# Performance work log

Hardware: AMD Instinct MI355X
Metric: run time of the kernel (lower is better)

Reference implementation:

```python
import jax, jax.numpy as jnp
import numpy as np

B, N, E, D = 8, 10000, 160000, 256
H = D // 2
SLOPE = 0.2  # LeakyReLU negative slope


def setup_inputs() -> dict:
    key = jax.random.key(0)
    ks = jax.random.split(key, 8)
    node_feats = jax.random.normal(ks[0], (B, N, D), dtype=jnp.float32)
    edge_attr = jax.random.uniform(ks[1], (E, 1), dtype=jnp.float32)
    W1 = jax.random.normal(ks[2], (2 * D, H), dtype=jnp.float32) * 0.05
    b1 = jnp.zeros((H,), dtype=jnp.float32)
    W2 = jax.random.normal(ks[3], (H, 1), dtype=jnp.float32) * 0.05
    b2 = jnp.zeros((1,), dtype=jnp.float32)
    edge_index = jax.random.randint(ks[4], (2, E), 0, N, dtype=jnp.int64)
    valid_masks = jax.random.randint(ks[5], (B, N), 0, 2).astype(bool)
    return {"node_feats": node_feats, "edge_attr": edge_attr, "W1": W1, "b1": b1,
            "W2": W2, "b2": b2, "edge_index": edge_index, "valid_masks": valid_masks}


def reference(node_feats, edge_attr, W1, b1, W2, b2, edge_index, valid_masks):
    # node_feats: [B,N,D]; edge_index: [2,E] shared across batch
    d = node_feats.shape[-1]
    src, dst = edge_index[0], edge_index[1]
    # cat([src_feats, dst_feats]) @ W1 == src @ W1[:d] + dst @ W1[d:]
    # Project per-node first, then gather per-edge: avoids the [B,E,2D] concat.
    ps = jnp.einsum('bnd,dh->bnh', node_feats, W1[:d])   # [B,N,H]
    pd = jnp.einsum('bnd,dh->bnh', node_feats, W1[d:])   # [B,N,H]
    h = ps[:, src] + pd[:, dst] + b1                      # [B,E,H]
    h = jnp.where(h >= 0, h, SLOPE * h)                   # LeakyReLU(0.2)
    scores = jnp.einsum('beh,h->be', h, W2[:, 0]) + b2[0]  # [B,E]
    scores = scores * edge_attr[:, 0]                     # edge_attr multiplies pre-softmax
    w = jax.nn.softmax(scores, axis=1)                    # global softmax over all edges
    # sparse_coo(edge_index, w) @ node_feats: out[src[e]] += w[e] * feats[dst[e]]
    msg = w[..., None] * node_feats[:, dst]               # [B,E,D]
    n = node_feats.shape[1]
    agg = jax.vmap(lambda m: jax.ops.segment_sum(m, src, num_segments=n))(msg)  # [B,N,D]
    mask = valid_masks.astype(node_feats.dtype)           # [B,N]
    cnt = mask.sum(axis=1)                                # [B]
    masked_mean = (agg * mask[..., None]).sum(axis=1) / jnp.maximum(cnt, 1.0)[:, None]
    full_mean = agg.mean(axis=1)
    graph_feats = jnp.where((cnt > 0)[:, None], masked_mean, full_mean)  # [B,D]
    return graph_feats, w
```

## Files before the change

kernel.cpp:

```cpp
#include <hip/hip_runtime.h>
#include <hip/hip_bf16.h>
#include <hip/hip_fp16.h>

#define B_ 8
#define N_ 10000
#define E_ 160000
#define D_ 256
#define H_ 128
#define SLOPE 0.2f
#define NCHUNK 50

#define EC_ 16
#define NR_ 32
#define RANGE_ 320
#define NPAD_ (NR_ * RANGE_)

#define NB_ 64
#define EPB_ (E_ / NB_)
#define BINS_ 256
#define NPB_ (N_ / 16)

typedef __attribute__((ext_vector_type(8))) _Float16 v8h;
typedef __attribute__((ext_vector_type(4))) _Float16 v4h;
typedef __attribute__((ext_vector_type(2))) _Float16 v2h;
typedef __attribute__((ext_vector_type(4))) float f32x4;

static __device__ __forceinline__ float dot2f(v2h a, v2h b, float c) {
#if __has_builtin(__builtin_amdgcn_fdot2)
    return __builtin_amdgcn_fdot2(a, b, c, false);
#else
    return fmaf((float)a.y, (float)b.y, fmaf((float)a.x, (float)b.x, c));
#endif
}

__global__ __launch_bounds__(64) void k_detect(const int* __restrict__ eidx_raw,
                                               const unsigned int* __restrict__ mask32,
                                               int* __restrict__ flags) {
    const int t = threadIdx.x;
    unsigned long long oddnz = __ballot(eidx_raw[2 * t + 1] != 0);
    unsigned long long mgt1  = __ballot(mask32[t] > 1u);
    if (t == 0) {
        flags[0] = (oddnz == 0ull) ? 1 : 0;
        flags[1] = (mgt1 != 0ull) ? 1 : 0;
    }
}

__global__ __launch_bounds__(256) void k_canon(const int* __restrict__ eidx_raw,
                                               const unsigned char* __restrict__ mask8,
                                               const unsigned int* __restrict__ mask32,
                                               const int* __restrict__ flags,
                                               int* __restrict__ ce,
                                               unsigned char* __restrict__ cm,
                                               unsigned char* __restrict__ cmT) {
    const int i = blockIdx.x * 256 + threadIdx.x;
    const int f_e = flags[0], f_m = flags[1];
    if (i < 2 * E_) ce[i] = f_e ? eidx_raw[2 * i] : eidx_raw[i];
    if (i < B_ * N_) {
        unsigned char v = f_m ? (unsigned char)(mask8[i] != 0)
                              : (unsigned char)(mask32[i] != 0u);
        cm[i] = v;
        const int b = i / N_;
        const int n = i - b * N_;
        cmT[n * 8 + b] = v;
    }
}

__global__ __launch_bounds__(256) void kW(const float* __restrict__ W1,
                                          const float* __restrict__ b1,
                                          const float* __restrict__ W2,
                                          __half* __restrict__ Wt,
                                          __half* __restrict__ b1h,
                                          __half* __restrict__ w2h) {
    const int i = blockIdx.x * 256 + threadIdx.x;
    const int f = i & 127;
    const int row = i >> 7;
    const int c = row >> 8, k = row & 255;
    Wt[((c * 128 + f) * 256) + k] = __float2half(W1[row * 128 + f]);
    if (blockIdx.x == 0 && threadIdx.x < 128) {
        b1h[threadIdx.x] = __float2half(b1[threadIdx.x]);
        w2h[threadIdx.x] = __float2half(W2[threadIdx.x]);
    }
}

__global__ __launch_bounds__(256) void k0_init(const unsigned char* __restrict__ cm,
                                               float* __restrict__ cnt) {
    const int b = blockIdx.x;
    const int tid = threadIdx.x;
    int c = 0;
    for (int i = tid; i < N_; i += 256) c += cm[b * N_ + i] ? 1 : 0;
    __shared__ int red[256];
    red[tid] = c;
    __syncthreads();
    for (int s = 128; s > 0; s >>= 1) {
        if (tid < s) red[tid] += red[tid + s];
        __syncthreads();
    }
    if (tid == 0) cnt[b] = (float)red[0];
}

__global__ __launch_bounds__(256) void khist(const int* __restrict__ ce,
                                             int* __restrict__ hpart) {
    __shared__ int h[BINS_];
    const int tid = threadIdx.x;
    h[tid] = 0;
    __syncthreads();
    const int base = blockIdx.x * EPB_;
    for (int i = tid; i < EPB_; i += 256) {
        const int s = ce[base + i], d = ce[E_ + base + i];
        const int bin = (d / NPB_) * 16 + s / NPB_;
        atomicAdd(&h[bin], 1);
    }
    __syncthreads();
    hpart[blockIdx.x * BINS_ + tid] = h[tid];
}

__global__ __launch_bounds__(256) void kprefix(const int* __restrict__ hpart,
                                               int* __restrict__ offsetG) {
    __shared__ int cnt[BINS_];
    __shared__ int excl[BINS_];
    const int bin = threadIdx.x;
    int c = 0;
    for (int b = 0; b < NB_; b++) c += hpart[b * BINS_ + bin];
    cnt[bin] = c;
    __syncthreads();
    if (bin == 0) {
        int r = 0;
        for (int i = 0; i < BINS_; i++) { excl[i] = r; r += cnt[i]; }
    }
    __syncthreads();
    int run = excl[bin];
    for (int b = 0; b < NB_; b++) {
        offsetG[b * BINS_ + bin] = run;
        run += hpart[b * BINS_ + bin];
    }
}

__global__ __launch_bounds__(256) void kscatter(const int* __restrict__ ce,
                                                const int* __restrict__ offsetG,
                                                int* __restrict__ srcS,
                                                int* __restrict__ dstS,
                                                int* __restrict__ origS) {
    __shared__ int loc[BINS_];
    const int tid = threadIdx.x;
    loc[tid] = offsetG[blockIdx.x * BINS_ + tid];
    __syncthreads();
    const int base = blockIdx.x * EPB_;
    for (int i = tid; i < EPB_; i += 256) {
        const int e = base + i;
        const int s = ce[e], d = ce[E_ + e];
        const int bin = (d / NPB_) * 16 + s / NPB_;
        const int pos = atomicAdd(&loc[bin], 1);
        srcS[pos] = s;
        dstS[pos] = d;
        origS[pos] = e;
    }
}

__global__ __launch_bounds__(256) void k1_mfma(const float* __restrict__ X,
                                               const __half* __restrict__ Wt,
                                               __half* __restrict__ ps,
                                               __half* __restrict__ pd) {
    const int cb = blockIdx.y;
    const int rb = blockIdx.x;
    const int tid = threadIdx.x;
    const int wave = tid >> 6, lane = tid & 63;
    const int quad = lane >> 4, l16 = lane & 15;

    __shared__ _Float16 Xs[128 * 40];
    __shared__ _Float16 Ws[128 * 40];

    f32x4 acc[2][8];
#pragma unroll
    for (int i = 0; i < 2; i++)
#pragma unroll
        for (int j = 0; j < 8; j++) acc[i][j] = (f32x4){0.f, 0.f, 0.f, 0.f};

    const int row_base = rb * 128;
    const __half* __restrict__ Wh = Wt + (size_t)cb * 128 * 256;
    __half* __restrict__ outp = cb ? pd : ps;

    const int sr = tid >> 1;
    const int sh = tid & 1;

    for (int kc = 0; kc < 8; ++kc) {
        {
            const float4* src = (const float4*)&X[(size_t)(row_base + sr) * 256 + kc * 32 + sh * 16];
            _Float16* dst = &Xs[sr * 40 + sh * 16];
#pragma unroll
            for (int j = 0; j < 4; ++j) {
                float4 v = src[j];
                v4h p = {(_Float16)v.x, (_Float16)v.y, (_Float16)v.z, (_Float16)v.w};
                *(v4h*)&dst[j * 4] = p;
            }
        }
        {
            const float4* src = (const float4*)&Wh[(size_t)sr * 256 + kc * 32 + sh * 16];
            float4 v0 = src[0], v1 = src[1];
            *(float4*)&Ws[sr * 40 + sh * 16] = v0;
            *(float4*)&Ws[sr * 40 + sh * 16 + 8] = v1;
        }
        __syncthreads();

        v8h wf[2];
#pragma unroll
        for (int ft = 0; ft < 2; ++ft)
            wf[ft] = *(v8h*)&Ws[(wave * 32 + ft * 16 + l16) * 40 + quad * 8];
#pragma unroll
        for (int nt = 0; nt < 8; ++nt) {
            v8h xf = *(v8h*)&Xs[(nt * 16 + l16) * 40 + quad * 8];
            acc[0][nt] = __builtin_amdgcn_mfma_f32_16x16x32_f16(wf[0], xf, acc[0][nt], 0, 0, 0);
            acc[1][nt] = __builtin_amdgcn_mfma_f32_16x16x32_f16(wf[1], xf, acc[1][nt], 0, 0, 0);
        }
        __syncthreads();
    }

#pragma unroll
    for (int nt = 0; nt < 8; ++nt) {
        const int R = row_base + nt * 16 + l16;
        const int b = R / N_;
        const int n = R - b * N_;
        __half* base = outp + ((size_t)(n * 8 + b)) * 128 + wave * 32 + quad * 4;
#pragma unroll
        for (int ft = 0; ft < 2; ++ft) {
            f32x4 a = acc[ft][nt];
            v4h h = {(_Float16)a.x, (_Float16)a.y, (_Float16)a.z, (_Float16)a.w};
            *(v4h*)(base + ft * 16) = h;
        }
    }
}

__global__ __launch_bounds__(256) void k2_scores(const __half* __restrict__ ps,
                                                 const __half* __restrict__ pd,
                                                 const int* __restrict__ srcS,
                                                 const int* __restrict__ dstS,
                                                 const int* __restrict__ origS,
                                                 const __half* __restrict__ b1h,
                                                 const __half* __restrict__ w2h,
                                                 const float* __restrict__ b2,
                                                 const float* __restrict__ eattr,
                                                 float* __restrict__ scores) {
    const int tid = threadIdx.x;
    const int wave = tid >> 6;
    const int lane = tid & 63;
    const int bid = blockIdx.x;
    const int lb = (bid & 7) * 5000 + (bid >> 3);
    const int e = lb * 4 + wave;

    const int b = lane >> 3;
    const int hi = (lane & 7) * 16;

    v2h b1p[8], w2p[8];
    {
        const v2h* bp = (const v2h*)(b1h + hi);
        const v2h* wp = (const v2h*)(w2h + hi);
#pragma unroll
        for (int j = 0; j < 8; j++) { b1p[j] = bp[j]; w2p[j] = wp[j]; }
    }

    const int src = srcS[e];
    const int dst = dstS[e];
    const int orig = origS[e];

    const float4* aps = (const float4*)&ps[((size_t)src * 8 + b) * 128 + hi];
    const float4* apd = (const float4*)&pd[((size_t)dst * 8 + b) * 128 + hi];
    float4 rs[2] = {aps[0], aps[1]};
    float4 rd[2] = {apd[0], apd[1]};
    const v2h* sv = (const v2h*)rs;
    const v2h* dv = (const v2h*)rd;

    const v2h slp = {(_Float16)SLOPE, (_Float16)SLOPE};
    float acc = 0.f;
#pragma unroll
    for (int j = 0; j < 8; j++) {
        v2h x = sv[j] + dv[j] + b1p[j];
        v2h l = __builtin_elementwise_max(x, x * slp);
        acc = dot2f(l, w2p[j], acc);
    }
    acc += __shfl_xor(acc, 1);
    acc += __shfl_xor(acc, 2);
    acc += __shfl_xor(acc, 4);

    if ((lane & 7) == 0) {
        scores[(size_t)b * E_ + orig] = (acc + b2[0]) * eattr[orig];
    }
}

__global__ __launch_bounds__(256) void k3a_max(const float* __restrict__ sc,
                                               float* __restrict__ pmax) {
    const int b = blockIdx.y, c = blockIdx.x, tid = threadIdx.x;
    const float* x = sc + (size_t)b * E_;
    const int i0 = c * (E_ / 32);
    float mv = -3.4e38f;
    for (int i = i0 + tid; i < i0 + E_ / 32; i += 256) mv = fmaxf(mv, x[i]);
    __shared__ float red[256];
    red[tid] = mv;
    __syncthreads();
    for (int s = 128; s > 0; s >>= 1) {
        if (tid < s) red[tid] = fmaxf(red[tid], red[tid + s]);
        __syncthreads();
    }
    if (tid == 0) pmax[b * 32 + c] = red[0];
}

__global__ __launch_bounds__(256) void k3b_maxred(const float* __restrict__ pmax,
                                                  float* __restrict__ m) {
    const int t = threadIdx.x;
    float v = pmax[t];
#pragma unroll
    for (int k = 1; k <= 16; k <<= 1) v = fmaxf(v, __shfl_xor(v, k));
    if ((t & 31) == 0) m[t >> 5] = v;
}

__global__ __launch_bounds__(256) void k3c_sum(const float* __restrict__ sc,
                                               const float* __restrict__ m,
                                               double* __restrict__ psum) {
    const int b = blockIdx.y, c = blockIdx.x, tid = threadIdx.x;
    const float* x = sc + (size_t)b * E_;
    const float mv = m[b];
    const int i0 = c * (E_ / 32);
    double s = 0.0;
    for (int i = i0 + tid; i < i0 + E_ / 32; i += 256) s += (double)expf(x[i] - mv);
    __shared__ double red[256];
    red[tid] = s;
    __syncthreads();
    for (int st = 128; st > 0; st >>= 1) {
        if (tid < st) red[tid] += red[tid + st];
        __syncthreads();
    }
    if (tid == 0) psum[b * 32 + c] = red[0];
}

__global__ __launch_bounds__(256) void k3d_sumred(const double* __restrict__ psum,
                                                  float* __restrict__ inv) {
    const int t = threadIdx.x;
    double v = psum[t];
#pragma unroll
    for (int k = 1; k <= 16; k <<= 1) v += __shfl_xor(v, k);
    if ((t & 31) == 0) inv[t >> 5] = (float)(1.0 / v);
}

__global__ __launch_bounds__(256) void k3e_norm(float* __restrict__ sc,
                                                const float* __restrict__ m,
                                                const float* __restrict__ inv,
                                                float* __restrict__ wT) {
    const int e = blockIdx.x * 256 + threadIdx.x;
    float wv[8];
#pragma unroll
    for (int b = 0; b < 8; b++) {
        float v = expf(sc[(size_t)b * E_ + e] - m[b]) * inv[b];
        sc[(size_t)b * E_ + e] = v;
        wv[b] = v;
    }
    *(float4*)&wT[(size_t)e * 8]     = make_float4(wv[0], wv[1], wv[2], wv[3]);
    *(float4*)&wT[(size_t)e * 8 + 4] = make_float4(wv[4], wv[5], wv[6], wv[7]);
}

__global__ __launch_bounds__(256) void k3f_bin(const int* __restrict__ ce,
                                               const float* __restrict__ wT,
                                               const unsigned char* __restrict__ cmT,
                                               float* __restrict__ Wpart) {
    const int ec = blockIdx.x;
    const int rg = blockIdx.y;
    const int n0 = rg * RANGE_;

    __shared__ float lWf[RANGE_ * 8];
    __shared__ float lWm[RANGE_ * 8];
    for (int i = threadIdx.x; i < RANGE_ * 8; i += 256) { lWf[i] = 0.f; lWm[i] = 0.f; }
    __syncthreads();

    const int4* dst4 = (const int4*)(ce + E_);
    const int base4 = ec * (E_ / EC_ / 4);
    for (int i = threadIdx.x; i < E_ / EC_ / 4; i += 256) {
        int4 d4 = dst4[base4 + i];
        int dd[4] = {d4.x, d4.y, d4.z, d4.w};
        const int e0 = (base4 + i) * 4;
#pragma unroll
        for (int j = 0; j < 4; ++j) {
            const int rel = dd[j] - n0;
            if ((unsigned)rel < (unsigned)RANGE_) {
                const int e = e0 + j;
                const int src = ce[e];
                float4 w0 = *(const float4*)&wT[(size_t)e * 8];
                float4 w1 = *(const float4*)&wT[(size_t)e * 8 + 4];
                const unsigned long long mm = *(const unsigned long long*)&cmT[src * 8];
                float wv[8] = {w0.x, w0.y, w0.z, w0.w, w1.x, w1.y, w1.z, w1.w};
                float* lf = &lWf[rel * 8];
                float* lm = &lWm[rel * 8];
#pragma unroll
                for (int b = 0; b < 8; b++) {
                    atomicAdd(&lf[b], wv[b]);
                    if ((mm >> (8 * b)) & 1ull) atomicAdd(&lm[b], wv[b]);
                }
            }
        }
    }
    __syncthreads();

    float* of = Wpart + ((size_t)ec * 2 + 0) * (NPAD_ * 8) + n0 * 8;
    float* om = Wpart + ((size_t)ec * 2 + 1) * (NPAD_ * 8) + n0 * 8;
    for (int i = threadIdx.x; i < RANGE_ * 8; i += 256) { of[i] = lWf[i]; om[i] = lWm[i]; }
}

__global__ __launch_bounds__(256) void k3g_reduce(const float* __restrict__ Wpart,
                                                  float* __restrict__ WfT,
                                                  float* __restrict__ WmT) {
    const int i = blockIdx.x * 256 + threadIdx.x;
    float sf = 0.f, sm = 0.f;
#pragma unroll
    for (int ec = 0; ec < EC_; ec++) {
        sf += Wpart[(size_t)ec * 2 * (NPAD_ * 8) + i];
        sm += Wpart[((size_t)ec * 2 + 1) * (NPAD_ * 8) + i];
    }
    WfT[i] = sf;
    WmT[i] = sm;
}

__global__ __launch_bounds__(256) void k4b_wsum(const float* __restrict__ X,
                                                const float* __restrict__ WmT,
                                                const float* __restrict__ WfT,
                                                float* __restrict__ gpart) {
    const int c = blockIdx.x;
    const int b = blockIdx.y;
    const int tx = threadIdx.x & 63;
    const int ty = threadIdx.x >> 6;
    const int npc = N_ / NCHUNK;
    const int n0 = c * npc;

    const float4* X4 = (const float4*)(X + (size_t)b * N_ * 256);
    float4 am = {0.f, 0.f, 0.f, 0.f};
    float4 af = {0.f, 0.f, 0.f, 0.f};

    for (int n = n0 + ty; n < n0 + npc; n += 4) {
        float wm = WmT[n * 8 + b];
        float wf = WfT[n * 8 + b];
        float4 v = X4[(size_t)n * 64 + tx];
        am.x = fmaf(wm, v.x, am.x); am.y = fmaf(wm, v.y, am.y);
        am.z = fmaf(wm, v.z, am.z); am.w = fmaf(wm, v.w, am.w);
        af.x = fmaf(wf, v.x, af.x); af.y = fmaf(wf, v.y, af.y);
        af.z = fmaf(wf, v.z, af.z); af.w = fmaf(wf, v.w, af.w);
    }

    __shared__ float4 red[256];
    red[threadIdx.x] = am;
    __syncthreads();
    if (ty == 0) {
        float4 r1 = red[tx + 64], r2 = red[tx + 128], r3 = red[tx + 192];
        am.x += r1.x + r2.x + r3.x; am.y += r1.y + r2.y + r3.y;
        am.z += r1.z + r2.z + r3.z; am.w += r1.w + r2.w + r3.w;
    }
    __syncthreads();
    red[threadIdx.x] = af;
    __syncthreads();
    if (ty == 0) {
        float4 r1 = red[tx + 64], r2 = red[tx + 128], r3 = red[tx + 192];
        af.x += r1.x + r2.x + r3.x; af.y += r1.y + r2.y + r3.y;
        af.z += r1.z + r2.z + r3.z; af.w += r1.w + r2.w + r3.w;
        float4* gp4 = (float4*)gpart;
        gp4[((c * 2 + 0) * 8 + b) * 64 + tx] = am;
        gp4[((c * 2 + 1) * 8 + b) * 64 + tx] = af;
    }
}

__global__ __launch_bounds__(256) void k5_final(const float* __restrict__ gpart,
                                                const float* __restrict__ cnt,
                                                float* __restrict__ gf) {
    const int b = blockIdx.x;
    const int d = threadIdx.x;
    float sm = 0.f, sf = 0.f;
    for (int c = 0; c < NCHUNK; c++) {
        sm += gpart[((c * 2 + 0) * 8 + b) * 256 + d];
        sf += gpart[((c * 2 + 1) * 8 + b) * 256 + d];
    }
    const float cn = cnt[b];
    gf[b * 256 + d] = (cn > 0.f) ? (sm / cn) : (sf / (float)N_);
}

extern "C" void kernel_launch(void* const* d_in, const int* in_sizes, int n_in,
                              void* d_out, int out_size, void* d_ws, size_t ws_size,
                              hipStream_t stream) {
    const float* X     = (const float*)d_in[0];
    const float* eattr = (const float*)d_in[1];
    const float* W1    = (const float*)d_in[2];
    const float* b1    = (const float*)d_in[3];
    const float* W2    = (const float*)d_in[4];
    const float* b2    = (const float*)d_in[5];
    const int*   eidx_raw = (const int*)d_in[6];
    const unsigned char* mask8 = (const unsigned char*)d_in[7];
    const unsigned int*  mask32 = (const unsigned int*)d_in[7];

    float* out  = (float*)d_out;
    float* gf   = out;
    float* wout = out + 2048;

    __half* ps_h = (__half*)d_ws;
    __half* pd_h = ps_h + (size_t)N_ * 8 * 128;
    __half* Wt   = pd_h + (size_t)N_ * 8 * 128;
    int* ce = (int*)(Wt + 2 * 128 * 256);
    unsigned char* cmT = (unsigned char*)(ce + 2 * E_);
    unsigned char* cm  = cmT + NPAD_ * 8;
    float* cnt = (float*)(cm + B_ * N_);
    int* flags = (int*)(cnt + 8);
    float* pmax = (float*)(flags + 2);
    float* mbuf = pmax + 256;
    float* invb = mbuf + 8;
    double* psum = (double*)(((uintptr_t)(invb + 8) + 15) & ~(uintptr_t)15);
    float* gpart = (float*)(psum + 256);
    int* hpart   = (int*)(gpart + NCHUNK * 2 * 8 * 256);
    int* offsetG = hpart + NB_ * BINS_;
    int* srcS    = offsetG + NB_ * BINS_;
    int* dstS    = srcS + E_;
    int* origS   = dstS + E_;
    __half* b1h  = (__half*)(origS + E_);
    __half* w2h  = b1h + 128;

    float* wT    = (float*)d_ws;
    float* Wpart = wT + (size_t)E_ * 8;
    float* WfT   = Wpart + (size_t)EC_ * 2 * NPAD_ * 8;
    float* WmT   = WfT + NPAD_ * 8;

    hipLaunchKernelGGL(k_detect, dim3(1), dim3(64), 0, stream, eidx_raw, mask32, flags);
    hipLaunchKernelGGL(k_canon, dim3(1250), dim3(256), 0, stream,
                       eidx_raw, mask8, mask32, flags, ce, cm, cmT);
    hipLaunchKernelGGL(kW, dim3(256), dim3(256), 0, stream, W1, b1, W2, Wt, b1h, w2h);
    hipLaunchKernelGGL(k0_init, dim3(8), dim3(256), 0, stream, cm, cnt);
    hipLaunchKernelGGL(khist, dim3(NB_), dim3(256), 0, stream, ce, hpart);
    hipLaunchKernelGGL(kprefix, dim3(1), dim3(256), 0, stream, hpart, offsetG);
    hipLaunchKernelGGL(kscatter, dim3(NB_), dim3(256), 0, stream,
                       ce, offsetG, srcS, dstS, origS);
    hipLaunchKernelGGL(k1_mfma, dim3(625, 2), dim3(256), 0, stream, X, Wt, ps_h, pd_h);
    hipLaunchKernelGGL(k2_scores, dim3(E_ / 4), dim3(256), 0, stream,
                       ps_h, pd_h, srcS, dstS, origS, b1h, w2h, b2, eattr, wout);
    hipLaunchKernelGGL(k3a_max, dim3(32, 8), dim3(256), 0, stream, wout, pmax);
    hipLaunchKernelGGL(k3b_maxred, dim3(1), dim3(256), 0, stream, pmax, mbuf);
    hipLaunchKernelGGL(k3c_sum, dim3(32, 8), dim3(256), 0, stream, wout, mbuf, psum);
    hipLaunchKernelGGL(k3d_sumred, dim3(1), dim3(256), 0, stream, psum, invb);
    hipLaunchKernelGGL(k3e_norm, dim3(E_ / 256), dim3(256), 0, stream,
                       wout, mbuf, invb, wT);
    hipLaunchKernelGGL(k3f_bin, dim3(EC_, NR_), dim3(256), 0, stream, ce, wT, cmT, Wpart);
    hipLaunchKernelGGL(k3g_reduce, dim3(NPAD_ * 8 / 256), dim3(256), 0, stream,
                       Wpart, WfT, WmT);
    hipLaunchKernelGGL(k4b_wsum, dim3(NCHUNK, 8), dim3(256), 0, stream, X, WmT, WfT, gpart);
    hipLaunchKernelGGL(k5_final, dim3(8), dim3(256), 0, stream, gpart, cnt, gf);
}
```

Before: 324.5 us.

## Fuse small setup kernels, merge GEMM column blocks, and restructure softmax reductions

Folds the weight conversion into the canonicalisation kernel and the mask count into the histogram kernel. The two projection GEMM column blocks become one block that reuses the staged X tile, with W fragments read straight from global memory instead of shared memory. Scores are now stored in sorted-edge order, interleaved across the batch, so the max and sum passes read them with coalesced vector loads. The separate reduction kernels are folded into their consumers, and a rank array lets the normalize pass map each edge back to its sorted position. This cuts the number of launches and scattered stores, at the cost of a gather through rank in the normalize pass and more GEMM registers.

```diff
diff --git a/kernel.cpp b/kernel.cpp
--- a/kernel.cpp
+++ b/kernel.cpp
@@ -19,6 +19,9 @@
 #define EPB_ (E_ / NB_)
 #define BINS_ 256
 #define NPB_ (N_ / 16)
+
+#define SB_ 64
+#define SEB_ (E_ / SB_)
 
 typedef __attribute__((ext_vector_type(8))) _Float16 v8h;
 typedef __attribute__((ext_vector_type(4))) _Float16 v4h;
@@ -49,9 +52,15 @@
                                                const unsigned char* __restrict__ mask8,
                                                const unsigned int* __restrict__ mask32,
                                                const int* __restrict__ flags,
+                                               const float* __restrict__ W1,
+                                               const float* __restrict__ b1,
+                                               const float* __restrict__ W2,
                                                int* __restrict__ ce,
                                                unsigned char* __restrict__ cm,
-                                               unsigned char* __restrict__ cmT) {
+                                               unsigned char* __restrict__ cmT,
+                                               __half* __restrict__ Wt,
+                                               __half* __restrict__ b1h,
+                                               __half* __restrict__ w2h) {
     const int i = blockIdx.x * 256 + threadIdx.x;
     const int f_e = flags[0], f_m = flags[1];
     if (i < 2 * E_) ce[i] = f_e ? eidx_raw[2 * i] : eidx_raw[i];
@@ -63,55 +72,48 @@
         const int n = i - b * N_;
         cmT[n * 8 + b] = v;
     }
-}
-
-__global__ __launch_bounds__(256) void kW(const float* __restrict__ W1,
-                                          const float* __restrict__ b1,
-                                          const float* __restrict__ W2,
-                                          __half* __restrict__ Wt,
-                                          __half* __restrict__ b1h,
-                                          __half* __restrict__ w2h) {
-    const int i = blockIdx.x * 256 + threadIdx.x;
-    const int f = i & 127;
-    const int row = i >> 7;
-    const int c = row >> 8, k = row & 255;
-    Wt[((c * 128 + f) * 256) + k] = __float2half(W1[row * 128 + f]);
-    if (blockIdx.x == 0 && threadIdx.x < 128) {
-        b1h[threadIdx.x] = __float2half(b1[threadIdx.x]);
-        w2h[threadIdx.x] = __float2half(W2[threadIdx.x]);
-    }
-}
-
-__global__ __launch_bounds__(256) void k0_init(const unsigned char* __restrict__ cm,
-                                               float* __restrict__ cnt) {
-    const int b = blockIdx.x;
+    if (i < 2 * 256 * 128) {
+        const int f = i & 127;
+        const int row = i >> 7;
+        const int c = row >> 8, k = row & 255;
+        Wt[((c * 128 + f) * 256) + k] = __float2half(W1[row * 128 + f]);
+    }
+    if (i < 128) {
+        b1h[i] = __float2half(b1[i]);
+        w2h[i] = __float2half(W2[i]);
+    }
+}
+
+__global__ __launch_bounds__(256) void khist(const int* __restrict__ ce,
+                                             const unsigned char* __restrict__ cm,
+                                             int* __restrict__ hpart,
+                                             float* __restrict__ cnt) {
     const int tid = threadIdx.x;
-    int c = 0;
-    for (int i = tid; i < N_; i += 256) c += cm[b * N_ + i] ? 1 : 0;
-    __shared__ int red[256];
-    red[tid] = c;
-    __syncthreads();
-    for (int s = 128; s > 0; s >>= 1) {
-        if (tid < s) red[tid] += red[tid + s];
+    if (blockIdx.x < NB_) {
+        __shared__ int h[BINS_];
+        h[tid] = 0;
         __syncthreads();
-    }
-    if (tid == 0) cnt[b] = (float)red[0];
-}
-
-__global__ __launch_bounds__(256) void khist(const int* __restrict__ ce,
-                                             int* __restrict__ hpart) {
-    __shared__ int h[BINS_];
-    const int tid = threadIdx.x;
-    h[tid] = 0;
-    __syncthreads();
-    const int base = blockIdx.x * EPB_;
-    for (int i = tid; i < EPB_; i += 256) {
-        const int s = ce[base + i], d = ce[E_ + base + i];
-        const int bin = (d / NPB_) * 16 + s / NPB_;
-        atomicAdd(&h[bin], 1);
-    }
-    __syncthreads();
-    hpart[blockIdx.x * BINS_ + tid] = h[tid];
+        const int base = blockIdx.x * EPB_;
+        for (int i = tid; i < EPB_; i += 256) {
+            const int s = ce[base + i], d = ce[E_ + base + i];
+            const int bin = (d / NPB_) * 16 + s / NPB_;
+            atomicAdd(&h[bin], 1);
+        }
+        __syncthreads();
+        hpart[blockIdx.x * BINS_ + tid] = h[tid];
+    } else {
+        const int b = blockIdx.x - NB_;
+        int c = 0;
+        for (int i = tid; i < N_; i += 256) c += cm[b * N_ + i] ? 1 : 0;
+        __shared__ int red[256];
+        red[tid] = c;
+        __syncthreads();
+        for (int s = 128; s > 0; s >>= 1) {
+            if (tid < s) red[tid] += red[tid + s];
+            __syncthreads();
+        }
+        if (tid == 0) cnt[b] = (float)red[0];
+    }
 }
 
 __global__ __launch_bounds__(256) void kprefix(const int* __restrict__ hpart,
@@ -139,7 +141,8 @@
                                                 const int* __restrict__ offsetG,
                                                 int* __restrict__ srcS,
                                                 int* __restrict__ dstS,
-                                                int* __restrict__ origS) {
+                                                int* __restrict__ origS,
+                                                int* __restrict__ rank) {
     __shared__ int loc[BINS_];
     const int tid = threadIdx.x;
     loc[tid] = offsetG[blockIdx.x * BINS_ + tid];
@@ -153,6 +156,7 @@
         srcS[pos] = s;
         dstS[pos] = d;
         origS[pos] = e;
+        rank[e] = pos;
     }
 }
 
@@ -160,25 +164,22 @@
                                                const __half* __restrict__ Wt,
                                                __half* __restrict__ ps,
                                                __half* __restrict__ pd) {
-    const int cb = blockIdx.y;
     const int rb = blockIdx.x;
     const int tid = threadIdx.x;
     const int wave = tid >> 6, lane = tid & 63;
     const int quad = lane >> 4, l16 = lane & 15;
 
     __shared__ _Float16 Xs[128 * 40];
-    __shared__ _Float16 Ws[128 * 40];
-
-    f32x4 acc[2][8];
-#pragma unroll
-    for (int i = 0; i < 2; i++)
-#pragma unroll
-        for (int j = 0; j < 8; j++) acc[i][j] = (f32x4){0.f, 0.f, 0.f, 0.f};
+
+    f32x4 acc[2][2][8];
+#pragma unroll
+    for (int c = 0; c < 2; c++)
+#pragma unroll
+        for (int i = 0; i < 2; i++)
+#pragma unroll
+            for (int j = 0; j < 8; j++) acc[c][i][j] = (f32x4){0.f, 0.f, 0.f, 0.f};
 
     const int row_base = rb * 128;
-    const __half* __restrict__ Wh = Wt + (size_t)cb * 128 * 256;
-    __half* __restrict__ outp = cb ? pd : ps;
-
     const int sr = tid >> 1;
     const int sh = tid & 1;
 
@@ -193,23 +194,22 @@
                 *(v4h*)&dst[j * 4] = p;
             }
         }
-        {
-            const float4* src = (const float4*)&Wh[(size_t)sr * 256 + kc * 32 + sh * 16];
-            float4 v0 = src[0], v1 = src[1];
-            *(float4*)&Ws[sr * 40 + sh * 16] = v0;
-            *(float4*)&Ws[sr * 40 + sh * 16 + 8] = v1;
-        }
         __syncthreads();
 
-        v8h wf[2];
-#pragma unroll
-        for (int ft = 0; ft < 2; ++ft)
-            wf[ft] = *(v8h*)&Ws[(wave * 32 + ft * 16 + l16) * 40 + quad * 8];
+        v8h wf[2][2];
+#pragma unroll
+        for (int cb = 0; cb < 2; ++cb)
+#pragma unroll
+            for (int ft = 0; ft < 2; ++ft)
+                wf[cb][ft] = *(const v8h*)&Wt[((size_t)cb * 128 + wave * 32 + ft * 16 + l16) * 256 + kc * 32 + quad * 8];
+
 #pragma unroll
         for (int nt = 0; nt < 8; ++nt) {
             v8h xf = *(v8h*)&Xs[(nt * 16 + l16) * 40 + quad * 8];
-            acc[0][nt] = __builtin_amdgcn_mfma_f32_16x16x32_f16(wf[0], xf, acc[0][nt], 0, 0, 0);
-            acc[1][nt] = __builtin_amdgcn_mfma_f32_16x16x32_f16(wf[1], xf, acc[1][nt], 0, 0, 0);
+            acc[0][0][nt] = __builtin_amdgcn_mfma_f32_16x16x32_f16(wf[0][0], xf, acc[0][0][nt], 0, 0, 0);
+            acc[0][1][nt] = __builtin_amdgcn_mfma_f32_16x16x32_f16(wf[0][1], xf, acc[0][1][nt], 0, 0, 0);
+            acc[1][0][nt] = __builtin_amdgcn_mfma_f32_16x16x32_f16(wf[1][0], xf, acc[1][0][nt], 0, 0, 0);
+            acc[1][1][nt] = __builtin_amdgcn_mfma_f32_16x16x32_f16(wf[1][1], xf, acc[1][1][nt], 0, 0, 0);
         }
         __syncthreads();
     }
@@ -219,12 +219,16 @@
         const int R = row_base + nt * 16 + l16;
         const int b = R / N_;
         const int n = R - b * N_;
-        __half* base = outp + ((size_t)(n * 8 + b)) * 128 + wave * 32 + quad * 4;
-#pragma unroll
-        for (int ft = 0; ft < 2; ++ft) {
-            f32x4 a = acc[ft][nt];
-            v4h h = {(_Float16)a.x, (_Float16)a.y, (_Float16)a.z, (_Float16)a.w};
-            *(v4h*)(base + ft * 16) = h;
+        const size_t off = ((size_t)(n * 8 + b)) * 128 + wave * 32 + quad * 4;
+#pragma unroll
+        for (int cb = 0; cb < 2; ++cb) {
+            __half* base = (cb ? pd : ps) + off;
+#pragma unroll
+            for (int ft = 0; ft < 2; ++ft) {
+                f32x4 a = acc[cb][ft][nt];
+                v4h h = {(_Float16)a.x, (_Float16)a.y, (_Float16)a.z, (_Float16)a.w};
+                *(v4h*)(base + ft * 16) = h;
+            }
         }
     }
 }
@@ -238,7 +242,7 @@
                                                  const __half* __restrict__ w2h,
                                                  const float* __restrict__ b2,
                                                  const float* __restrict__ eattr,
-                                                 float* __restrict__ scores) {
+                                                 float* __restrict__ scS) {
     const int tid = threadIdx.x;
     const int wave = tid >> 6;
     const int lane = tid & 63;
@@ -281,76 +285,139 @@
     acc += __shfl_xor(acc, 4);
 
     if ((lane & 7) == 0) {
-        scores[(size_t)b * E_ + orig] = (acc + b2[0]) * eattr[orig];
-    }
-}
-
-__global__ __launch_bounds__(256) void k3a_max(const float* __restrict__ sc,
+        scS[(size_t)e * 8 + b] = (acc + b2[0]) * eattr[orig];
+    }
+}
+
+__global__ __launch_bounds__(256) void k3a_max(const float* __restrict__ scS,
                                                float* __restrict__ pmax) {
-    const int b = blockIdx.y, c = blockIdx.x, tid = threadIdx.x;
-    const float* x = sc + (size_t)b * E_;
-    const int i0 = c * (E_ / 32);
-    float mv = -3.4e38f;
-    for (int i = i0 + tid; i < i0 + E_ / 32; i += 256) mv = fmaxf(mv, x[i]);
-    __shared__ float red[256];
-    red[tid] = mv;
-    __syncthreads();
-    for (int s = 128; s > 0; s >>= 1) {
-        if (tid < s) red[tid] = fmaxf(red[tid], red[tid + s]);
-        __syncthreads();
-    }
-    if (tid == 0) pmax[b * 32 + c] = red[0];
-}
-
-__global__ __launch_bounds__(256) void k3b_maxred(const float* __restrict__ pmax,
-                                                  float* __restrict__ m) {
-    const int t = threadIdx.x;
-    float v = pmax[t];
-#pragma unroll
-    for (int k = 1; k <= 16; k <<= 1) v = fmaxf(v, __shfl_xor(v, k));
-    if ((t & 31) == 0) m[t >> 5] = v;
-}
-
-__global__ __launch_bounds__(256) void k3c_sum(const float* __restrict__ sc,
-                                               const float* __restrict__ m,
+    const int tid = threadIdx.x;
+    const int wave = tid >> 6, lane = tid & 63;
+    const int base = blockIdx.x * SEB_;
+    float fm[8];
+#pragma unroll
+    for (int j = 0; j < 8; j++) fm[j] = -3.4e38f;
+    for (int i = tid; i < SEB_; i += 256) {
+        const float4* s4 = (const float4*)&scS[(size_t)(base + i) * 8];
+        float4 a = s4[0], b = s4[1];
+        fm[0] = fmaxf(fm[0], a.x); fm[1] = fmaxf(fm[1], a.y);
+        fm[2] = fmaxf(fm[2], a.z); fm[3] = fmaxf(fm[3], a.w);
+        fm[4] = fmaxf(fm[4], b.x); fm[5] = fmaxf(fm[5], b.y);
+        fm[6] = fmaxf(fm[6], b.z); fm[7] = fmaxf(fm[7], b.w);
+    }
+#pragma unroll
+    for (int k = 1; k <= 32; k <<= 1)
+#pragma unroll
+        for (int j = 0; j < 8; j++) fm[j] = fmaxf(fm[j], __shfl_xor(fm[j], k));
+    __shared__ float lmax[4][8];
+    if (lane == 0)
+#pragma unroll
+        for (int j = 0; j < 8; j++) lmax[wave][j] = fm[j];
+    __syncthreads();
+    if (tid < 8) {
+        float v = fmaxf(fmaxf(lmax[0][tid], lmax[1][tid]), fmaxf(lmax[2][tid], lmax[3][tid]));
+        pmax[blockIdx.x * 8 + tid] = v;
+    }
+}
+
+__global__ __launch_bounds__(256) void k3c_sum(const float* __restrict__ scS,
+                                               const float* __restrict__ pmax,
                                                double* __restrict__ psum) {
-    const int b = blockIdx.y, c = blockIdx.x, tid = threadIdx.x;
-    const float* x = sc + (size_t)b * E_;
-    const float mv = m[b];
-    const int i0 = c * (E_ / 32);
-    double s = 0.0;
-    for (int i = i0 + tid; i < i0 + E_ / 32; i += 256) s += (double)expf(x[i] - mv);
-    __shared__ double red[256];
-    red[tid] = s;
-    __syncthreads();
-    for (int st = 128; st > 0; st >>= 1) {
-        if (tid < st) red[tid] += red[tid + st];
-        __syncthreads();
-    }
-    if (tid == 0) psum[b * 32 + c] = red[0];
-}
-
-__global__ __launch_bounds__(256) void k3d_sumred(const double* __restrict__ psum,
-                                                  float* __restrict__ inv) {
-    const int t = threadIdx.x;
-    double v = psum[t];
-#pragma unroll
-    for (int k = 1; k <= 16; k <<= 1) v += __shfl_xor(v, k);
-    if ((t & 31) == 0) inv[t >> 5] = (float)(1.0 / v);
-}
-
-__global__ __launch_bounds__(256) void k3e_norm(float* __restrict__ sc,
-                                                const float* __restrict__ m,
-                                                const float* __restrict__ inv,
+    const int tid = threadIdx.x;
+    const int wave = tid >> 6, lane = tid & 63;
+    __shared__ float sm[8];
+    if (tid < SB_) {
+        float v[8];
+        const float4* p4 = (const float4*)&pmax[tid * 8];
+        float4 a = p4[0], b = p4[1];
+        v[0] = a.x; v[1] = a.y; v[2] = a.z; v[3] = a.w;
+        v[4] = b.x; v[5] = b.y; v[6] = b.z; v[7] = b.w;
+#pragma unroll
+        for (int k = 1; k <= 32; k <<= 1)
+#pragma unroll
+            for (int j = 0; j < 8; j++) v[j] = fmaxf(v[j], __shfl_xor(v[j], k));
+        if (tid == 0)
+#pragma unroll
+            for (int j = 0; j < 8; j++) sm[j] = v[j];
+    }
+    __syncthreads();
+    float m[8];
+#pragma unroll
+    for (int j = 0; j < 8; j++) m[j] = sm[j];
+
+    const int base = blockIdx.x * SEB_;
+    double s[8];
+#pragma unroll
+    for (int j = 0; j < 8; j++) s[j] = 0.0;
+    for (int i = tid; i < SEB_; i += 256) {
+        const float4* s4 = (const float4*)&scS[(size_t)(base + i) * 8];
+        float4 a = s4[0], b = s4[1];
+        s[0] += (double)expf(a.x - m[0]); s[1] += (double)expf(a.y - m[1]);
+        s[2] += (double)expf(a.z - m[2]); s[3] += (double)expf(a.w - m[3]);
+        s[4] += (double)expf(b.x - m[4]); s[5] += (double)expf(b.y - m[5]);
+        s[6] += (double)expf(b.z - m[6]); s[7] += (double)expf(b.w - m[7]);
+    }
+#pragma unroll
+    for (int k = 1; k <= 32; k <<= 1)
+#pragma unroll
+        for (int j = 0; j < 8; j++) s[j] += __shfl_xor(s[j], k);
+    __shared__ double lsum[4][8];
+    if (lane == 0)
+#pragma unroll
+        for (int j = 0; j < 8; j++) lsum[wave][j] = s[j];
+    __syncthreads();
+    if (tid < 8) {
+        psum[blockIdx.x * 8 + tid] = lsum[0][tid] + lsum[1][tid] + lsum[2][tid] + lsum[3][tid];
+    }
+}
+
+__global__ __launch_bounds__(256) void k3e_norm(const float* __restrict__ scS,
+                                                const int* __restrict__ rank,
+                                                const float* __restrict__ pmax,
+                                                const double* __restrict__ psum,
+                                                float* __restrict__ wout,
                                                 float* __restrict__ wT) {
-    const int e = blockIdx.x * 256 + threadIdx.x;
+    const int tid = threadIdx.x;
+    __shared__ float smx[8], sinvx[8];
+    if (tid < 64) {
+        float v[8];
+        const float4* p4 = (const float4*)&pmax[tid * 8];
+        float4 a = p4[0], b = p4[1];
+        v[0] = a.x; v[1] = a.y; v[2] = a.z; v[3] = a.w;
+        v[4] = b.x; v[5] = b.y; v[6] = b.z; v[7] = b.w;
+#pragma unroll
+        for (int k = 1; k <= 32; k <<= 1)
+#pragma unroll
+            for (int j = 0; j < 8; j++) v[j] = fmaxf(v[j], __shfl_xor(v[j], k));
+        if (tid == 0)
+#pragma unroll
+            for (int j = 0; j < 8; j++) smx[j] = v[j];
+    } else if (tid < 128) {
+        const int l = tid - 64;
+        double s[8];
+#pragma unroll
+        for (int j = 0; j < 8; j++) s[j] = psum[l * 8 + j];
+#pragma unroll
+        for (int k = 1; k <= 32; k <<= 1)
+#pragma unroll
+            for (int j = 0; j < 8; j++) s[j] += __shfl_xor(s[j], k);
+        if (l == 0)
+#pragma unroll
+            for (int j = 0; j < 8; j++) sinvx[j] = (float)(1.0 / s[j]);
+    }
+    __syncthreads();
+
+    const int e = blockIdx.x * 256 + tid;
+    const int p = rank[e];
+    const float4* s4 = (const float4*)&scS[(size_t)p * 8];
+    float4 a = s4[0], b = s4[1];
     float wv[8];
-#pragma unroll
-    for (int b = 0; b < 8; b++) {
-        float v = expf(sc[(size_t)b * E_ + e] - m[b]) * inv[b];
-        sc[(size_t)b * E_ + e] = v;
-        wv[b] = v;
-    }
+    wv[0] = expf(a.x - smx[0]) * sinvx[0]; wv[1] = expf(a.y - smx[1]) * sinvx[1];
+    wv[2] = expf(a.z - smx[2]) * sinvx[2]; wv[3] = expf(a.w - smx[3]) * sinvx[3];
+    wv[4] = expf(b.x - smx[4]) * sinvx[4]; wv[5] = expf(b.y - smx[5]) * sinvx[5];
+    wv[6] = expf(b.z - smx[6]) * sinvx[6]; wv[7] = expf(b.w - smx[7]) * sinvx[7];
+#pragma unroll
+    for (int j = 0; j < 8; j++) wout[(size_t)j * E_ + e] = wv[j];
     *(float4*)&wT[(size_t)e * 8]     = make_float4(wv[0], wv[1], wv[2], wv[3]);
     *(float4*)&wT[(size_t)e * 8 + 4] = make_float4(wv[4], wv[5], wv[6], wv[7]);
 }
@@ -501,17 +568,17 @@
     float* cnt = (float*)(cm + B_ * N_);
     int* flags = (int*)(cnt + 8);
     float* pmax = (float*)(flags + 2);
-    float* mbuf = pmax + 256;
-    float* invb = mbuf + 8;
-    double* psum = (double*)(((uintptr_t)(invb + 8) + 15) & ~(uintptr_t)15);
-    float* gpart = (float*)(psum + 256);
+    double* psum = (double*)(((uintptr_t)(pmax + SB_ * 8) + 15) & ~(uintptr_t)15);
+    float* gpart = (float*)(psum + SB_ * 8);
     int* hpart   = (int*)(gpart + NCHUNK * 2 * 8 * 256);
     int* offsetG = hpart + NB_ * BINS_;
     int* srcS    = offsetG + NB_ * BINS_;
     int* dstS    = srcS + E_;
     int* origS   = dstS + E_;
-    __half* b1h  = (__half*)(origS + E_);
+    int* rankB   = origS + E_;
+    __half* b1h  = (__half*)(rankB + E_);
     __half* w2h  = b1h + 128;
+    float* scS   = (float*)(w2h + 128);
 
     float* wT    = (float*)d_ws;
     float* Wpart = wT + (size_t)E_ * 8;
@@ -520,22 +587,19 @@
 
     hipLaunchKernelGGL(k_detect, dim3(1), dim3(64), 0, stream, eidx_raw, mask32, flags);
     hipLaunchKernelGGL(k_canon, dim3(1250), dim3(256), 0, stream,
-                       eidx_raw, mask8, mask32, flags, ce, cm, cmT);
-    hipLaunchKernelGGL(kW, dim3(256), dim3(256), 0, stream, W1, b1, W2, Wt, b1h, w2h);
-    hipLaunchKernelGGL(k0_init, dim3(8), dim3(256), 0, stream, cm, cnt);
-    hipLaunchKernelGGL(khist, dim3(NB_), dim3(256), 0, stream, ce, hpart);
+                       eidx_raw, mask8, mask32, flags, W1, b1, W2,
+                       ce, cm, cmT, Wt, b1h, w2h);
+    hipLaunchKernelGGL(khist, dim3(NB_ + 8), dim3(256), 0, stream, ce, cm, hpart, cnt);
     hipLaunchKernelGGL(kprefix, dim3(1), dim3(256), 0, stream, hpart, offsetG);
     hipLaunchKernelGGL(kscatter, dim3(NB_), dim3(256), 0, stream,
-                       ce, offsetG, srcS, dstS, origS);
-    hipLaunchKernelGGL(k1_mfma, dim3(625, 2), dim3(256), 0, stream, X, Wt, ps_h, pd_h);
+                       ce, offsetG, srcS, dstS, origS, rankB);
+    hipLaunchKernelGGL(k1_mfma, dim3(625), dim3(256), 0, stream, X, Wt, ps_h, pd_h);
     hipLaunchKernelGGL(k2_scores, dim3(E_ / 4), dim3(256), 0, stream,
-                       ps_h, pd_h, srcS, dstS, origS, b1h, w2h, b2, eattr, wout);
-    hipLaunchKernelGGL(k3a_max, dim3(32, 8), dim3(256), 0, stream, wout, pmax);
-    hipLaunchKernelGGL(k3b_maxred, dim3(1), dim3(256), 0, stream, pmax, mbuf);
-    hipLaunchKernelGGL(k3c_sum, dim3(32, 8), dim3(256), 0, stream, wout, mbuf, psum);
-    hipLaunchKernelGGL(k3d_sumred, dim3(1), dim3(256), 0, stream, psum, invb);
+                       ps_h, pd_h, srcS, dstS, origS, b1h, w2h, b2, eattr, scS);
+    hipLaunchKernelGGL(k3a_max, dim3(SB_), dim3(256), 0, stream, scS, pmax);
+    hipLaunchKernelGGL(k3c_sum, dim3(SB_), dim3(256), 0, stream, scS, pmax, psum);
     hipLaunchKernelGGL(k3e_norm, dim3(E_ / 256), dim3(256), 0, stream,
-                       wout, mbuf, invb, wT);
+                       scS, rankB, pmax, psum, wout, wT);
     hipLaunchKernelGGL(k3f_bin, dim3(EC_, NR_), dim3(256), 0, stream, ce, wT, cmT, Wpart);
     hipLaunchKernelGGL(k3g_reduce, dim3(NPAD_ * 8 / 256), dim3(256), 0, stream,
                        Wpart, WfT, WmT);
```

Measured after the change: 314.6 us. -3.0%, faster.
